# Performance work log

Hardware: AMD Instinct MI355X
Metric: run time of the kernel (lower is better)

The kernel has to match this reference:

```python
import jax, jax.numpy as jnp
import numpy as np

HEADS = 4


def setup_inputs() -> dict:
    key = jax.random.key(0)
    ks = jax.random.split(key, 5)
    B, T, C, H, W = 2, 16, 256, 64, 64
    x = jax.random.normal(ks[0], (B, T, C, H, W), dtype=jnp.float32)
    s = 1.0 / np.sqrt(C).astype(np.float32)  # kaiming-ish init scale for 1x1 conv
    Wq = jax.random.normal(ks[1], (C, C), dtype=jnp.float32) * s
    Wk = jax.random.normal(ks[2], (C, C), dtype=jnp.float32) * s
    Wv = jax.random.normal(ks[3], (C, C), dtype=jnp.float32) * s
    Wp = jax.random.normal(ks[4], (C, C), dtype=jnp.float32) * s
    return {"x": x, "Wq": Wq, "Wk": Wk, "Wv": Wv, "Wp": Wp}


def reference(x, Wq, Wk, Wv, Wp):
    B, T, C, H, W = x.shape
    heads = HEADS
    Ch = C // heads
    scale = Ch ** (-0.5)
    # [B,T,C,H,W] -> [B*H*W, T, C]: each spatial pixel has a T x C temporal track
    xf = jnp.transpose(x, (0, 3, 4, 1, 2)).reshape(B * H * W, T, C)
    # Conv1d(C,C,1,bias=False) == channel matmul: out[n,t,d] = sum_c W[d,c] x[n,t,c]
    q = jnp.einsum('ntc,dc->ntd', xf, Wq).reshape(-1, T, heads, Ch) * scale
    k = jnp.einsum('ntc,dc->ntd', xf, Wk).reshape(-1, T, heads, Ch)
    v = jnp.einsum('ntc,dc->ntd', xf, Wv).reshape(-1, T, heads, Ch)
    k_soft = jax.nn.softmax(k, axis=1)    # softmax over time T (torch dim=-1 of [n,h,c,t])
    q_soft = jax.nn.softmax(q, axis=-1)   # softmax over head channels Ch (torch dim=-2)
    # linear attention: outer-product context then query contraction
    kv = jnp.einsum('nthc,nthd->nhcd', k_soft, v)         # [N,h,Ch,Ch]
    out = jnp.einsum('nthc,nhcd->nthd', q_soft, kv)       # [N,T,h,Ch]
    out = out.reshape(-1, T, C)
    out = jnp.einsum('ntc,dc->ntd', out, Wp)
    out = out.reshape(B, H, W, T, C)
    return jnp.transpose(out, (0, 3, 4, 1, 2))
```

## Files before the change

### kernel.cpp

```cpp
#include <hip/hip_runtime.h>
#include <hip/hip_bf16.h>

#define DI __device__ __forceinline__

typedef __attribute__((ext_vector_type(8))) short bf16x8;
typedef __attribute__((ext_vector_type(4))) float f32x4;
typedef __attribute__((ext_vector_type(4))) _Float16 f16x4;

constexpr int XPAD = 264;
constexpr float LOG2E = 1.4426950408889634f;

DI short f2bf(float f) {
  __hip_bfloat16 h = __float2bfloat16(f);
  union { __hip_bfloat16 h; short s; } c; c.h = h; return c.s;
}

DI unsigned pk2(float a, float b) {
  union { __hip_bfloat162 h; unsigned u; } c;
  c.h.x = __float2bfloat16(a); c.h.y = __float2bfloat16(b);
  return c.u;
}

DI f16x4 pkh4(float a, float b, float c, float d) {
  auto lo = __builtin_amdgcn_cvt_pkrtz(a, b);
  auto hi = __builtin_amdgcn_cvt_pkrtz(c, d);
  union { struct { decltype(lo) l, h; } p; f16x4 v; } u;
  u.p.l = lo; u.p.h = hi;
  return u.v;
}

DI f32x4 mfma16(bf16x8 a, bf16x8 b, f32x4 c) {
  return __builtin_amdgcn_mfma_f32_16x16x32_bf16(a, b, c, 0, 0, 0);
}

DI f32x4 mfmah(f16x4 a, f16x4 b, f32x4 c) {
  return __builtin_amdgcn_mfma_f32_16x16x16f16(a, b, c, 0, 0, 0);
}

DI f32x4 fzero() { return f32x4{0.f, 0.f, 0.f, 0.f}; }

DI int xsw(int row, int e) { return row * 256 + (e ^ ((row & 7) << 3)); }

__global__ void wconv_kernel(const float* __restrict__ a, const float* __restrict__ b,
                             const float* __restrict__ c, const float* __restrict__ d,
                             short* __restrict__ o) {
  int i = blockIdx.x * 256 + threadIdx.x;
  int mat = i >> 14;
  int off = (i & 16383) * 4;
  const float* s = (mat == 0) ? a : (mat == 1) ? b : (mat == 2) ? c : d;
  const float sc = (mat == 0) ? 0.125f : 1.0f;
  float4 v = *(const float4*)(s + off);
  uint2 r; r.x = pk2(v.x * sc, v.y * sc); r.y = pk2(v.z * sc, v.w * sc);
  *(uint2*)(o + mat * 65536 + off) = r;
}

__global__ __launch_bounds__(256, 4)
void k1_kernel(const float* __restrict__ x, const short* __restrict__ wbf,
               short* __restrict__ att, short* __restrict__ qsg, int n0chunk) {
  __shared__ short SMEM[16384];
  short* Xs = SMEM;

  const int tid  = threadIdx.x;
  const int wave = tid >> 6;
  const int lane = tid & 63;
  const int g    = lane >> 4;
  const int li   = lane & 15;

  short* kvt = SMEM + wave * 2560;

  int bid = blockIdx.x;
  const int nb = gridDim.x;
  if ((nb & 7) == 0) { const int q = nb >> 3; bid = (bid & 7) * q + (bid >> 3); }

  const int n0  = n0chunk + bid * 4;
  const int b   = n0 >> 12;
  const int hw0 = n0 & 4095;
  const float* xb = x + (size_t)b * (16 * 256 * 4096) + hw0;

  {
    const int c4 = lane;
    #pragma unroll
    for (int it = 0; it < 4; ++it) {
      const int t = it * 4 + wave;
      const float* src = xb + (size_t)(t * 256 + c4 * 4) * 4096;
      float4 v0 = *(const float4*)(src);
      float4 v1 = *(const float4*)(src + 4096);
      float4 v2 = *(const float4*)(src + 8192);
      float4 v3 = *(const float4*)(src + 12288);
      uint2 s0; s0.x = pk2(v0.x, v1.x); s0.y = pk2(v2.x, v3.x);
      uint2 s1; s1.x = pk2(v0.y, v1.y); s1.y = pk2(v2.y, v3.y);
      uint2 s2; s2.x = pk2(v0.z, v1.z); s2.y = pk2(v2.z, v3.z);
      uint2 s3; s3.x = pk2(v0.w, v1.w); s3.y = pk2(v2.w, v3.w);
      *(uint2*)&Xs[xsw(0 * 16 + t, c4 * 4)] = s0;
      *(uint2*)&Xs[xsw(1 * 16 + t, c4 * 4)] = s1;
      *(uint2*)&Xs[xsw(2 * 16 + t, c4 * 4)] = s2;
      *(uint2*)&Xs[xsw(3 * 16 + t, c4 * 4)] = s3;
    }
  }
  __syncthreads();

  const short* wq = wbf;
  const short* wk = wbf + 65536;
  const short* wv = wbf + 131072;
  const size_t wrow = (size_t)(wave * 64) * 256;

  {
    f32x4 qacc[4][4];
    #pragma unroll
    for (int p = 0; p < 4; ++p)
      #pragma unroll
      for (int nt = 0; nt < 4; ++nt) qacc[p][nt] = fzero();

    __builtin_amdgcn_s_setprio(1);
    #pragma unroll
    for (int ks = 0; ks < 8; ++ks) {
      bf16x8 qb[4];
      #pragma unroll
      for (int nt = 0; nt < 4; ++nt)
        qb[nt] = *(const bf16x8*)(wq + wrow + (size_t)(nt * 16 + li) * 256 + ks * 32 + g * 8);
      #pragma unroll
      for (int p = 0; p < 4; ++p) {
        bf16x8 af = *(const bf16x8*)&Xs[xsw(p * 16 + li, ks * 32 + g * 8)];
        #pragma unroll
        for (int nt = 0; nt < 4; ++nt)
          qacc[p][nt] = mfma16(af, qb[nt], qacc[p][nt]);
      }
    }
    __builtin_amdgcn_s_setprio(0);

    #pragma unroll
    for (int p = 0; p < 4; ++p) {
      short* qsp = qsg + (size_t)(bid * 4 + p) * 4096;
      #pragma unroll
      for (int r = 0; r < 4; ++r) {
        float e0 = exp2f(qacc[p][0][r] * LOG2E);
        float e1 = exp2f(qacc[p][1][r] * LOG2E);
        float e2 = exp2f(qacc[p][2][r] * LOG2E);
        float e3 = exp2f(qacc[p][3][r] * LOG2E);
        float s = e0 + e1 + e2 + e3;
        s += __shfl_xor(s, 1); s += __shfl_xor(s, 2);
        s += __shfl_xor(s, 4); s += __shfl_xor(s, 8);
        const float inv = 1.f / s;
        const int t = g * 4 + r;
        short* dst = qsp + t * 256 + wave * 64 + li;
        dst[0]  = f2bf(e0 * inv);
        dst[16] = f2bf(e1 * inv);
        dst[32] = f2bf(e2 * inv);
        dst[48] = f2bf(e3 * inv);
      }
    }
  }

  f16x4 akf[4][4];
  {
    f32x4 kacc[4][4];
    #pragma unroll
    for (int p = 0; p < 4; ++p)
      #pragma unroll
      for (int nt = 0; nt < 4; ++nt) kacc[p][nt] = fzero();

    __builtin_amdgcn_s_setprio(1);
    #pragma unroll
    for (int ks = 0; ks < 8; ++ks) {
      bf16x8 kb[4];
      #pragma unroll
      for (int nt = 0; nt < 4; ++nt)
        kb[nt] = *(const bf16x8*)(wk + wrow + (size_t)(nt * 16 + li) * 256 + ks * 32 + g * 8);
      #pragma unroll
      for (int p = 0; p < 4; ++p) {
        bf16x8 af = *(const bf16x8*)&Xs[xsw(p * 16 + li, ks * 32 + g * 8)];
        #pragma unroll
        for (int nt = 0; nt < 4; ++nt)
          kacc[p][nt] = mfma16(af, kb[nt], kacc[p][nt]);
      }
    }
    __builtin_amdgcn_s_setprio(0);

    #pragma unroll
    for (int p = 0; p < 4; ++p)
      #pragma unroll
      for (int nt = 0; nt < 4; ++nt) {
        float e0 = exp2f(kacc[p][nt][0] * LOG2E);
        float e1 = exp2f(kacc[p][nt][1] * LOG2E);
        float e2 = exp2f(kacc[p][nt][2] * LOG2E);
        float e3 = exp2f(kacc[p][nt][3] * LOG2E);
        float s = e0 + e1 + e2 + e3;
        s += __shfl_xor(s, 16);
        s += __shfl_xor(s, 32);
        const float inv = 1.f / s;
        akf[p][nt] = pkh4(e0 * inv, e1 * inv, e2 * inv, e3 * inv);
      }
  }

  f16x4 bvf[4][4];
  #pragma unroll
  for (int h = 0; h < 2; ++h) {
    f32x4 vacc[4][2];
    #pragma unroll
    for (int p = 0; p < 4; ++p)
      #pragma unroll
      for (int n2 = 0; n2 < 2; ++n2) vacc[p][n2] = fzero();

    __builtin_amdgcn_s_setprio(1);
    #pragma unroll
    for (int ks = 0; ks < 8; ++ks) {
      bf16x8 vb[2];
      #pragma unroll
      for (int n2 = 0; n2 < 2; ++n2)
        vb[n2] = *(const bf16x8*)(wv + wrow + (size_t)((h * 2 + n2) * 16 + li) * 256 + ks * 32 + g * 8);
      #pragma unroll
      for (int p = 0; p < 4; ++p) {
        bf16x8 af = *(const bf16x8*)&Xs[xsw(p * 16 + li, ks * 32 + g * 8)];
        #pragma unroll
        for (int n2 = 0; n2 < 2; ++n2)
          vacc[p][n2] = mfma16(af, vb[n2], vacc[p][n2]);
      }
    }
    __builtin_amdgcn_s_setprio(0);

    #pragma unroll
    for (int p = 0; p < 4; ++p)
      #pragma unroll
      for (int n2 = 0; n2 < 2; ++n2)
        bvf[p][h * 2 + n2] = pkh4(vacc[p][n2][0], vacc[p][n2][1],
                                  vacc[p][n2][2], vacc[p][n2][3]);
  }

  __syncthreads();

  #pragma unroll
  for (int p = 0; p < 4; ++p) {
    const short* qsp = qsg + (size_t)(bid * 4 + p) * 4096;
    f32x4 oacc[4];
    #pragma unroll
    for (int nt = 0; nt < 4; ++nt) oacc[nt] = fzero();

    #pragma unroll
    for (int cc = 0; cc < 2; ++cc) {
      #pragma unroll
      for (int cm = 0; cm < 2; ++cm) {
        f32x4 kva[4];
        #pragma unroll
        for (int nt = 0; nt < 4; ++nt) kva[nt] = fzero();
        #pragma unroll
        for (int nt = 0; nt < 4; ++nt)
          kva[nt] = mfmah(akf[p][cc * 2 + cm], bvf[p][nt], kva[nt]);
        #pragma unroll
        for (int nt = 0; nt < 4; ++nt) {
          uint2 s4;
          s4.x = pk2(kva[nt][0], kva[nt][1]);
          s4.y = pk2(kva[nt][2], kva[nt][3]);
          *(uint2*)&kvt[(nt * 16 + li) * 40 + cm * 16 + g * 4] = s4;
        }
      }
      bf16x8 aq = *(const bf16x8*)(qsp + li * 256 + wave * 64 + cc * 32 + g * 8);
      #pragma unroll
      for (int nt = 0; nt < 4; ++nt) {
        bf16x8 bq = *(const bf16x8*)&kvt[(nt * 16 + li) * 40 + g * 8];
        oacc[nt] = mfma16(aq, bq, oacc[nt]);
      }
    }

    const size_t arow = ((size_t)bid * 4 + p) * 16;
    #pragma unroll
    for (int nt = 0; nt < 4; ++nt)
      #pragma unroll
      for (int r = 0; r < 4; ++r)
        att[(arow + g * 4 + r) * 256 + wave * 64 + nt * 16 + li] = f2bf(oacc[nt][r]);
  }
}

__global__ __launch_bounds__(256, 2)
void k2_kernel(const short* __restrict__ att, const short* __restrict__ wpb,
               float* __restrict__ out, int n0chunk) {
  __shared__ short A[128 * XPAD];
  const int tid = threadIdx.x;
  const int wave = tid >> 6, lane = tid & 63, g = lane >> 4, li = lane & 15;
  const int pb = blockIdx.x >> 1;
  const int t0 = (blockIdx.x & 1) * 8;
  const int n0 = n0chunk + pb * 16;
  const int b = n0 >> 12, hw0 = n0 & 4095;

  for (int idx = tid; idx < 128 * 32; idx += 256) {
    const int row = idx >> 5, seg = idx & 31;
    const int p = row & 15, tl = row >> 4;
    const short* src = att + ((size_t)((pb * 16 + p) * 16 + t0 + tl)) * 256 + seg * 8;
    *(int4*)&A[row * XPAD + seg * 8] = *(const int4*)src;
  }
  __syncthreads();

  f32x4 acc[8][4];
  #pragma unroll
  for (int mt = 0; mt < 8; ++mt)
    #pragma unroll
    for (int n4 = 0; n4 < 4; ++n4) acc[mt][n4] = fzero();

  #pragma unroll
  for (int ks = 0; ks < 8; ++ks) {
    bf16x8 bf[4];
    #pragma unroll
    for (int n4 = 0; n4 < 4; ++n4)
      bf[n4] = *(const bf16x8*)(wpb + (size_t)((wave * 4 + n4) * 16 + li) * 256 + ks * 32 + g * 8);
    #pragma unroll
    for (int mt = 0; mt < 8; ++mt) {
      bf16x8 af = *(const bf16x8*)&A[(mt * 16 + li) * XPAD + ks * 32 + g * 8];
      #pragma unroll
      for (int n4 = 0; n4 < 4; ++n4) acc[mt][n4] = mfma16(af, bf[n4], acc[mt][n4]);
    }
  }

  float* ob = out + (size_t)b * (16 * 256 * 4096) + hw0;
  #pragma unroll
  for (int mt = 0; mt < 8; ++mt)
    #pragma unroll
    for (int n4 = 0; n4 < 4; ++n4) {
      const int t = t0 + mt;
      const int c = (wave * 4 + n4) * 16 + li;
      float4 v;
      v.x = acc[mt][n4][0]; v.y = acc[mt][n4][1];
      v.z = acc[mt][n4][2]; v.w = acc[mt][n4][3];
      *(float4*)(ob + (size_t)(t * 256 + c) * 4096 + g * 4) = v;
    }
}

extern "C" void kernel_launch(void* const* d_in, const int* in_sizes, int n_in,
                              void* d_out, int out_size, void* d_ws, size_t ws_size,
                              hipStream_t stream) {
  const float* x  = (const float*)d_in[0];
  const float* Wq = (const float*)d_in[1];
  const float* Wk = (const float*)d_in[2];
  const float* Wv = (const float*)d_in[3];
  const float* Wp = (const float*)d_in[4];
  float* out = (float*)d_out;

  short* wbf = (short*)d_ws;
  short* att = wbf + 4 * 65536;

  wconv_kernel<<<256, 256, 0, stream>>>(Wq, Wk, Wv, Wp, wbf);

  const size_t wsAvail = (ws_size > 524288) ? (ws_size - 524288) : 0;
  const size_t perPix = 16 * 256 * 2;
  int chunk = 16;
  while (chunk < 8192 && (size_t)(chunk * 2) * perPix <= wsAvail) chunk <<= 1;

  short* qsg = att + (size_t)chunk * 4096;

  for (int n0 = 0; n0 < 8192; n0 += chunk) {
    k1_kernel<<<chunk / 4, 256, 0, stream>>>(x, wbf, att, qsg, n0);
    k2_kernel<<<(chunk / 16) * 2, 256, 0, stream>>>(att, wbf + 3 * 65536, out, n0);
  }
}
```

Measured before the change: 242.5 us.

## Split x transpose into pre-pass kernel and keep q softmax in LDS

Adds a separate transpose kernel that converts x to bf16 in the pre-swizzled per-pixel layout, so k1 can fill shared memory with direct global-to-LDS loads instead of strided fp32 gathers. The Q projection is moved after K/V and its softmax result is kept in a per-wave LDS tile in fp16, which removes the global qsg round trip and a block barrier. The kv context now feeds the output MFMA straight from registers as fp16 rather than going through LDS. The cost is an extra kernel launch per chunk and an extra bf16 write and read of the whole x tensor. Occupancy drops from 4 to 3 blocks per CU.

```diff
diff --git a/kernel.cpp b/kernel.cpp
--- a/kernel.cpp
+++ b/kernel.cpp
@@ -19,6 +19,11 @@
   union { __hip_bfloat162 h; unsigned u; } c;
   c.h.x = __float2bfloat16(a); c.h.y = __float2bfloat16(b);
   return c.u;
+}
+
+DI short f2h(float f) {
+  _Float16 h = (_Float16)f;
+  union { _Float16 h; short s; } c; c.h = h; return c.s;
 }
 
 DI f16x4 pkh4(float a, float b, float c, float d) {
@@ -27,6 +32,12 @@
   union { struct { decltype(lo) l, h; } p; f16x4 v; } u;
   u.p.l = lo; u.p.h = hi;
   return u.v;
+}
+
+DI f16x4 ld4h(const short* p) {
+  union { uint2 u; f16x4 v; } c;
+  c.u = *(const uint2*)p;
+  return c.v;
 }
 
 DI f32x4 mfma16(bf16x8 a, bf16x8 b, f32x4 c) {
@@ -54,10 +65,49 @@
   *(uint2*)(o + mat * 65536 + off) = r;
 }
 
-__global__ __launch_bounds__(256, 4)
-void k1_kernel(const float* __restrict__ x, const short* __restrict__ wbf,
-               short* __restrict__ att, short* __restrict__ qsg, int n0chunk) {
-  __shared__ short SMEM[16384];
+__global__ __launch_bounds__(256, 2)
+void xt_kernel(const float* __restrict__ x, short* __restrict__ xt, int n0chunk) {
+  __shared__ short T[64 * 258];
+  const int tid = threadIdx.x;
+  const int gi  = blockIdx.x >> 4;
+  const int t   = blockIdx.x & 15;
+  const int n0g = n0chunk + gi * 64;
+  const int b   = n0g >> 12;
+  const int hw0 = n0g & 4095;
+  const float* xb = x + ((size_t)(b * 16 + t) * 256) * 4096 + hw0;
+
+  #pragma unroll
+  for (int ci = 0; ci < 16; ++ci) {
+    const int c   = ci * 16 + (tid >> 4);
+    const int px4 = tid & 15;
+    float4 v = *(const float4*)(xb + (size_t)c * 4096 + px4 * 4);
+    T[(px4 * 4 + 0) * 258 + c] = f2bf(v.x);
+    T[(px4 * 4 + 1) * 258 + c] = f2bf(v.y);
+    T[(px4 * 4 + 2) * 258 + c] = f2bf(v.z);
+    T[(px4 * 4 + 3) * 258 + c] = f2bf(v.w);
+  }
+  __syncthreads();
+
+  const int wave = tid >> 6, lane = tid & 63;
+  #pragma unroll
+  for (int itp = 0; itp < 16; ++itp) {
+    const int px  = itp * 4 + wave;
+    const int row = (px & 3) * 16 + t;
+    const int sw8 = (row & 7) << 3;
+    const size_t obase = ((size_t)(gi * 16 + (px >> 2))) * 16384 + row * 256;
+    const int dstc = (((lane >> 1) * 8) ^ sw8) + (lane & 1) * 4;
+    const int tb = px * 258 + lane * 4;
+    union { short s[4]; uint2 u; } pk;
+    pk.s[0] = T[tb + 0]; pk.s[1] = T[tb + 1];
+    pk.s[2] = T[tb + 2]; pk.s[3] = T[tb + 3];
+    *(uint2*)&xt[obase + dstc] = pk.u;
+  }
+}
+
+__global__ __launch_bounds__(256, 3)
+void k1_kernel(const short* __restrict__ xt, const short* __restrict__ wbf,
+               short* __restrict__ att) {
+  __shared__ short SMEM[16384 + 4096];
   short* Xs = SMEM;
 
   const int tid  = threadIdx.x;
@@ -66,35 +116,20 @@
   const int g    = lane >> 4;
   const int li   = lane & 15;
 
-  short* kvt = SMEM + wave * 2560;
+  short* qs = SMEM + 16384 + wave * 1024;
 
   int bid = blockIdx.x;
   const int nb = gridDim.x;
   if ((nb & 7) == 0) { const int q = nb >> 3; bid = (bid & 7) * q + (bid >> 3); }
 
-  const int n0  = n0chunk + bid * 4;
-  const int b   = n0 >> 12;
-  const int hw0 = n0 & 4095;
-  const float* xb = x + (size_t)b * (16 * 256 * 4096) + hw0;
-
   {
-    const int c4 = lane;
-    #pragma unroll
-    for (int it = 0; it < 4; ++it) {
-      const int t = it * 4 + wave;
-      const float* src = xb + (size_t)(t * 256 + c4 * 4) * 4096;
-      float4 v0 = *(const float4*)(src);
-      float4 v1 = *(const float4*)(src + 4096);
-      float4 v2 = *(const float4*)(src + 8192);
-      float4 v3 = *(const float4*)(src + 12288);
-      uint2 s0; s0.x = pk2(v0.x, v1.x); s0.y = pk2(v2.x, v3.x);
-      uint2 s1; s1.x = pk2(v0.y, v1.y); s1.y = pk2(v2.y, v3.y);
-      uint2 s2; s2.x = pk2(v0.z, v1.z); s2.y = pk2(v2.z, v3.z);
-      uint2 s3; s3.x = pk2(v0.w, v1.w); s3.y = pk2(v2.w, v3.w);
-      *(uint2*)&Xs[xsw(0 * 16 + t, c4 * 4)] = s0;
-      *(uint2*)&Xs[xsw(1 * 16 + t, c4 * 4)] = s1;
-      *(uint2*)&Xs[xsw(2 * 16 + t, c4 * 4)] = s2;
-      *(uint2*)&Xs[xsw(3 * 16 + t, c4 * 4)] = s3;
+    const short* src = xt + (size_t)bid * 16384 + wave * 512 + lane * 8;
+    #pragma unroll
+    for (int it = 0; it < 8; ++it) {
+      __builtin_amdgcn_global_load_lds(
+          (const __attribute__((address_space(1))) void*)(src + it * 2048),
+          (__attribute__((address_space(3))) void*)(SMEM + it * 2048 + wave * 512),
+          16, 0, 0);
     }
   }
   __syncthreads();
@@ -103,53 +138,6 @@
   const short* wk = wbf + 65536;
   const short* wv = wbf + 131072;
   const size_t wrow = (size_t)(wave * 64) * 256;
-
-  {
-    f32x4 qacc[4][4];
-    #pragma unroll
-    for (int p = 0; p < 4; ++p)
-      #pragma unroll
-      for (int nt = 0; nt < 4; ++nt) qacc[p][nt] = fzero();
-
-    __builtin_amdgcn_s_setprio(1);
-    #pragma unroll
-    for (int ks = 0; ks < 8; ++ks) {
-      bf16x8 qb[4];
-      #pragma unroll
-      for (int nt = 0; nt < 4; ++nt)
-        qb[nt] = *(const bf16x8*)(wq + wrow + (size_t)(nt * 16 + li) * 256 + ks * 32 + g * 8);
-      #pragma unroll
-      for (int p = 0; p < 4; ++p) {
-        bf16x8 af = *(const bf16x8*)&Xs[xsw(p * 16 + li, ks * 32 + g * 8)];
-        #pragma unroll
-        for (int nt = 0; nt < 4; ++nt)
-          qacc[p][nt] = mfma16(af, qb[nt], qacc[p][nt]);
-      }
-    }
-    __builtin_amdgcn_s_setprio(0);
-
-    #pragma unroll
-    for (int p = 0; p < 4; ++p) {
-      short* qsp = qsg + (size_t)(bid * 4 + p) * 4096;
-      #pragma unroll
-      for (int r = 0; r < 4; ++r) {
-        float e0 = exp2f(qacc[p][0][r] * LOG2E);
-        float e1 = exp2f(qacc[p][1][r] * LOG2E);
-        float e2 = exp2f(qacc[p][2][r] * LOG2E);
-        float e3 = exp2f(qacc[p][3][r] * LOG2E);
-        float s = e0 + e1 + e2 + e3;
-        s += __shfl_xor(s, 1); s += __shfl_xor(s, 2);
-        s += __shfl_xor(s, 4); s += __shfl_xor(s, 8);
-        const float inv = 1.f / s;
-        const int t = g * 4 + r;
-        short* dst = qsp + t * 256 + wave * 64 + li;
-        dst[0]  = f2bf(e0 * inv);
-        dst[16] = f2bf(e1 * inv);
-        dst[32] = f2bf(e2 * inv);
-        dst[48] = f2bf(e3 * inv);
-      }
-    }
-  }
 
   f16x4 akf[4][4];
   {
@@ -226,38 +214,65 @@
                                   vacc[p][n2][2], vacc[p][n2][3]);
   }
 
-  __syncthreads();
+  f32x4 qacc[4][4];
+  #pragma unroll
+  for (int p = 0; p < 4; ++p)
+    #pragma unroll
+    for (int nt = 0; nt < 4; ++nt) qacc[p][nt] = fzero();
+
+  __builtin_amdgcn_s_setprio(1);
+  #pragma unroll
+  for (int ks = 0; ks < 8; ++ks) {
+    bf16x8 qb[4];
+    #pragma unroll
+    for (int nt = 0; nt < 4; ++nt)
+      qb[nt] = *(const bf16x8*)(wq + wrow + (size_t)(nt * 16 + li) * 256 + ks * 32 + g * 8);
+    #pragma unroll
+    for (int p = 0; p < 4; ++p) {
+      bf16x8 af = *(const bf16x8*)&Xs[xsw(p * 16 + li, ks * 32 + g * 8)];
+      #pragma unroll
+      for (int nt = 0; nt < 4; ++nt)
+        qacc[p][nt] = mfma16(af, qb[nt], qacc[p][nt]);
+    }
+  }
+  __builtin_amdgcn_s_setprio(0);
 
   #pragma unroll
   for (int p = 0; p < 4; ++p) {
-    const short* qsp = qsg + (size_t)(bid * 4 + p) * 4096;
+    #pragma unroll
+    for (int r = 0; r < 4; ++r) {
+      float e0 = exp2f(qacc[p][0][r] * LOG2E);
+      float e1 = exp2f(qacc[p][1][r] * LOG2E);
+      float e2 = exp2f(qacc[p][2][r] * LOG2E);
+      float e3 = exp2f(qacc[p][3][r] * LOG2E);
+      float s = e0 + e1 + e2 + e3;
+      s += __shfl_xor(s, 1); s += __shfl_xor(s, 2);
+      s += __shfl_xor(s, 4); s += __shfl_xor(s, 8);
+      const float inv = 1.f / s;
+      const int t = g * 4 + r;
+      const int xw = (t & 7) << 3;
+      short* dq = qs + t * 64;
+      dq[( 0 + li) ^ xw] = f2h(e0 * inv);
+      dq[(16 + li) ^ xw] = f2h(e1 * inv);
+      dq[(32 + li) ^ xw] = f2h(e2 * inv);
+      dq[(48 + li) ^ xw] = f2h(e3 * inv);
+    }
+
     f32x4 oacc[4];
     #pragma unroll
     for (int nt = 0; nt < 4; ++nt) oacc[nt] = fzero();
 
     #pragma unroll
-    for (int cc = 0; cc < 2; ++cc) {
-      #pragma unroll
-      for (int cm = 0; cm < 2; ++cm) {
-        f32x4 kva[4];
-        #pragma unroll
-        for (int nt = 0; nt < 4; ++nt) kva[nt] = fzero();
-        #pragma unroll
-        for (int nt = 0; nt < 4; ++nt)
-          kva[nt] = mfmah(akf[p][cc * 2 + cm], bvf[p][nt], kva[nt]);
-        #pragma unroll
-        for (int nt = 0; nt < 4; ++nt) {
-          uint2 s4;
-          s4.x = pk2(kva[nt][0], kva[nt][1]);
-          s4.y = pk2(kva[nt][2], kva[nt][3]);
-          *(uint2*)&kvt[(nt * 16 + li) * 40 + cm * 16 + g * 4] = s4;
-        }
-      }
-      bf16x8 aq = *(const bf16x8*)(qsp + li * 256 + wave * 64 + cc * 32 + g * 8);
+    for (int cq = 0; cq < 4; ++cq) {
+      f32x4 kva[4];
+      #pragma unroll
+      for (int nt = 0; nt < 4; ++nt)
+        kva[nt] = mfmah(akf[p][cq], bvf[p][nt], fzero());
+      f16x4 aq = ld4h(qs + li * 64 + (((cq * 16 + g * 4) ^ ((li & 7) << 3))));
       #pragma unroll
       for (int nt = 0; nt < 4; ++nt) {
-        bf16x8 bq = *(const bf16x8*)&kvt[(nt * 16 + li) * 40 + g * 8];
-        oacc[nt] = mfma16(aq, bq, oacc[nt]);
+        f16x4 kb16 = pkh4(kva[nt][0], kva[nt][1], kva[nt][2], kva[nt][3]);
+        oacc[nt] = mfmah(aq, kb16, oacc[nt]);
       }
     }
 
@@ -340,13 +355,14 @@
 
   const size_t wsAvail = (ws_size > 524288) ? (ws_size - 524288) : 0;
   const size_t perPix = 16 * 256 * 2;
-  int chunk = 16;
+  int chunk = 64;
   while (chunk < 8192 && (size_t)(chunk * 2) * perPix <= wsAvail) chunk <<= 1;
 
-  short* qsg = att + (size_t)chunk * 4096;
+  short* xt = att + (size_t)chunk * 4096;
 
   for (int n0 = 0; n0 < 8192; n0 += chunk) {
-    k1_kernel<<<chunk / 4, 256, 0, stream>>>(x, wbf, att, qsg, n0);
+    xt_kernel<<<(chunk / 64) * 16, 256, 0, stream>>>(x, xt, n0);
+    k1_kernel<<<chunk / 4, 256, 0, stream>>>(xt, wbf, att);
     k2_kernel<<<(chunk / 16) * 2, 256, 0, stream>>>(att, wbf + 3 * 65536, out, n0);
   }
 }
```

After: 245.9 us. About the same (+1.4%).

## Keep kv context in registers and switch q-softmax scratch to per-wave fp16

Applied to the files above, without the earlier changes.

The kv outer-product tile is no longer written through LDS and re-read. Each 16-wide chunk of the MFMA result is packed to fp16 in registers and fed straight into a 16x16x16 f16 MFMA with the query operand. The query-softmax scratch moves to a per-wave fp16 layout, so the block barrier becomes a wave-local vmcnt wait. Exp and reciprocal use the hardware intrinsics directly. This drops LDS traffic and the block sync, at the cost of fp16 precision for q_soft and kv and relying on ordered same-wave global write then read.

```diff
diff --git a/kernel.cpp b/kernel.cpp
--- a/kernel.cpp
+++ b/kernel.cpp
@@ -9,6 +9,9 @@
 
 constexpr int XPAD = 264;
 constexpr float LOG2E = 1.4426950408889634f;
+
+DI float fexp(float x) { return __builtin_amdgcn_exp2f(x * LOG2E); }
+DI float frcp(float x) { return __builtin_amdgcn_rcpf(x); }
 
 DI short f2bf(float f) {
   __hip_bfloat16 h = __float2bfloat16(f);
@@ -19,6 +22,11 @@
   union { __hip_bfloat162 h; unsigned u; } c;
   c.h.x = __float2bfloat16(a); c.h.y = __float2bfloat16(b);
   return c.u;
+}
+
+DI short f2h(float f) {
+  _Float16 h = (_Float16)f;
+  union { _Float16 h; short s; } c; c.h = h; return c.s;
 }
 
 DI f16x4 pkh4(float a, float b, float c, float d) {
@@ -27,6 +35,12 @@
   union { struct { decltype(lo) l, h; } p; f16x4 v; } u;
   u.p.l = lo; u.p.h = hi;
   return u.v;
+}
+
+DI f16x4 ld4h(const short* p) {
+  union { uint2 u; f16x4 v; } c;
+  c.u = *(const uint2*)p;
+  return c.v;
 }
 
 DI f32x4 mfma16(bf16x8 a, bf16x8 b, f32x4 c) {
@@ -65,8 +79,6 @@
   const int lane = tid & 63;
   const int g    = lane >> 4;
   const int li   = lane & 15;
-
-  short* kvt = SMEM + wave * 2560;
 
   int bid = blockIdx.x;
   const int nb = gridDim.x;
@@ -103,6 +115,7 @@
   const short* wk = wbf + 65536;
   const short* wv = wbf + 131072;
   const size_t wrow = (size_t)(wave * 64) * 256;
+  short* qsw = qsg + ((size_t)bid * 4 * 4 + wave) * 1024;
 
   {
     f32x4 qacc[4][4];
@@ -130,23 +143,23 @@
 
     #pragma unroll
     for (int p = 0; p < 4; ++p) {
-      short* qsp = qsg + (size_t)(bid * 4 + p) * 4096;
+      short* qsp = qsw + p * 4096;
       #pragma unroll
       for (int r = 0; r < 4; ++r) {
-        float e0 = exp2f(qacc[p][0][r] * LOG2E);
-        float e1 = exp2f(qacc[p][1][r] * LOG2E);
-        float e2 = exp2f(qacc[p][2][r] * LOG2E);
-        float e3 = exp2f(qacc[p][3][r] * LOG2E);
+        float e0 = fexp(qacc[p][0][r]);
+        float e1 = fexp(qacc[p][1][r]);
+        float e2 = fexp(qacc[p][2][r]);
+        float e3 = fexp(qacc[p][3][r]);
         float s = e0 + e1 + e2 + e3;
         s += __shfl_xor(s, 1); s += __shfl_xor(s, 2);
         s += __shfl_xor(s, 4); s += __shfl_xor(s, 8);
-        const float inv = 1.f / s;
+        const float inv = frcp(s);
         const int t = g * 4 + r;
-        short* dst = qsp + t * 256 + wave * 64 + li;
-        dst[0]  = f2bf(e0 * inv);
-        dst[16] = f2bf(e1 * inv);
-        dst[32] = f2bf(e2 * inv);
-        dst[48] = f2bf(e3 * inv);
+        short* dst = qsp + t * 64 + li;
+        dst[0]  = f2h(e0 * inv);
+        dst[16] = f2h(e1 * inv);
+        dst[32] = f2h(e2 * inv);
+        dst[48] = f2h(e3 * inv);
       }
     }
   }
@@ -180,14 +193,14 @@
     for (int p = 0; p < 4; ++p)
       #pragma unroll
       for (int nt = 0; nt < 4; ++nt) {
-        float e0 = exp2f(kacc[p][nt][0] * LOG2E);
-        float e1 = exp2f(kacc[p][nt][1] * LOG2E);
-        float e2 = exp2f(kacc[p][nt][2] * LOG2E);
-        float e3 = exp2f(kacc[p][nt][3] * LOG2E);
+        float e0 = fexp(kacc[p][nt][0]);
+        float e1 = fexp(kacc[p][nt][1]);
+        float e2 = fexp(kacc[p][nt][2]);
+        float e3 = fexp(kacc[p][nt][3]);
         float s = e0 + e1 + e2 + e3;
         s += __shfl_xor(s, 16);
         s += __shfl_xor(s, 32);
-        const float inv = 1.f / s;
+        const float inv = frcp(s);
         akf[p][nt] = pkh4(e0 * inv, e1 * inv, e2 * inv, e3 * inv);
       }
   }
@@ -226,38 +239,26 @@
                                   vacc[p][n2][2], vacc[p][n2][3]);
   }
 
-  __syncthreads();
+  asm volatile("s_waitcnt vmcnt(0)" ::: "memory");
 
   #pragma unroll
   for (int p = 0; p < 4; ++p) {
-    const short* qsp = qsg + (size_t)(bid * 4 + p) * 4096;
+    const short* qsp = qsw + p * 4096;
     f32x4 oacc[4];
     #pragma unroll
     for (int nt = 0; nt < 4; ++nt) oacc[nt] = fzero();
 
     #pragma unroll
-    for (int cc = 0; cc < 2; ++cc) {
-      #pragma unroll
-      for (int cm = 0; cm < 2; ++cm) {
-        f32x4 kva[4];
-        #pragma unroll
-        for (int nt = 0; nt < 4; ++nt) kva[nt] = fzero();
-        #pragma unroll
-        for (int nt = 0; nt < 4; ++nt)
-          kva[nt] = mfmah(akf[p][cc * 2 + cm], bvf[p][nt], kva[nt]);
-        #pragma unroll
-        for (int nt = 0; nt < 4; ++nt) {
-          uint2 s4;
-          s4.x = pk2(kva[nt][0], kva[nt][1]);
-          s4.y = pk2(kva[nt][2], kva[nt][3]);
-          *(uint2*)&kvt[(nt * 16 + li) * 40 + cm * 16 + g * 4] = s4;
-        }
-      }
-      bf16x8 aq = *(const bf16x8*)(qsp + li * 256 + wave * 64 + cc * 32 + g * 8);
+    for (int cq = 0; cq < 4; ++cq) {
+      f32x4 kva[4];
+      #pragma unroll
+      for (int nt = 0; nt < 4; ++nt)
+        kva[nt] = mfmah(akf[p][cq], bvf[p][nt], fzero());
+      f16x4 aq = ld4h(qsp + li * 64 + cq * 16 + g * 4);
       #pragma unroll
       for (int nt = 0; nt < 4; ++nt) {
-        bf16x8 bq = *(const bf16x8*)&kvt[(nt * 16 + li) * 40 + g * 8];
-        oacc[nt] = mfma16(aq, bq, oacc[nt]);
+        f16x4 kb16 = pkh4(kva[nt][0], kva[nt][1], kva[nt][2], kva[nt][3]);
+        oacc[nt] = mfmah(aq, kb16, oacc[nt]);
       }
     }
 
```

New measurement: 242.4 us. No clear change (-0.1%).
